# Kernel tuning notes

Hardware: AMD Instinct MI355X
Metric: run time of the kernel (lower is better)

The kernel has to match this reference:

```python
import jax, jax.numpy as jnp
import numpy as np
from jax.scipy.special import logsumexp

B, T, V, C, H, D, SPW, NC = 16, 256, 10000, 4096, 256, 256, 32, 128


def _res(x, w1, b1, w2, b2):
    # ResLayer: x + relu(lin2(relu(lin1(x))))
    return x + jax.nn.relu(jax.nn.relu(x @ w1 + b1) @ w2 + b2)


def _log_phi(x, proj):
    # Performer-style log random features for the softmax kernel (smp param.)
    return x @ proj - 0.5 * jnp.sum(x * x, -1, keepdims=True)


def _log_matmul_exp(a, b):
    # logits[i,j] = logsumexp_d(a[i,d] + b[j,d]), stable, via a single GEMM
    ma = jnp.max(a, -1, keepdims=True)
    mb = jnp.max(b, -1, keepdims=True)
    return jnp.log(jnp.exp(a - ma) @ jnp.exp(b - mb).T) + ma + mb.T


def setup_inputs() -> dict:
    key = jax.random.key(0)
    ks = jax.random.split(key, 12)
    s = 1.0 / np.sqrt(H)  # xavier-ish scale
    inp = {
        "text": jax.random.randint(ks[0], (B, T), 0, V),
        "start_emb": jax.random.normal(ks[1], (H,), jnp.float32) * s,
        "start_w": jax.random.normal(ks[2], (5, H, H), jnp.float32) * s,
        "start_b": jnp.zeros((5, H), jnp.float32),
        "state_emb": jax.random.normal(ks[3], (C, H), jnp.float32) * s,
        "next_state_emb": jax.random.normal(ks[4], (C, H), jnp.float32) * s,
        "preterminal_emb": jax.random.normal(ks[5], (C, H), jnp.float32) * s,
        "terminal_w": jax.random.normal(ks[6], (4, H, H), jnp.float32) * s,
        "terminal_b": jnp.zeros((4, H), jnp.float32),
        "terminal_emb": jax.random.normal(ks[7], (V, H), jnp.float32) * s,
        "projection": jax.random.normal(ks[8], (H, D), jnp.float32),
    }
    # brown-cluster style assignment: each cluster owns SPW disjoint states
    w2c = jax.random.randint(ks[9], (V,), 0, NC)
    c2s = jnp.arange(NC)[:, None] * SPW + jnp.arange(SPW)[None, :]
    inp["word2state"] = c2s[w2c]  # [V, SPW]
    return inp


def reference(text, word2state, start_emb, start_w, start_b, state_emb,
              next_state_emb, preterminal_emb, terminal_w, terminal_b,
              terminal_emb, projection):
    # --- start distribution (tie_start=True uses next_state_emb) ---
    fx = start_emb @ start_w[0] + start_b[0]
    fx = _res(fx, start_w[1], start_b[1], start_w[2], start_b[2])
    fx = _res(fx, start_w[3], start_b[3], start_w[4], start_b[4])
    lpy = _log_phi(next_state_emb, projection)                      # [C, D]
    start_lp = jax.nn.log_softmax(
        _log_matmul_exp(_log_phi(fx[None], projection), lpy)[0])    # [C]
    # --- transition: kernelized low-rank logits, row log-softmax ---
    trans_lp = jax.nn.log_softmax(
        _log_matmul_exp(_log_phi(state_emb, projection), lpy), -1)  # [C, C]
    # --- emission: terminal_mlp + sparse word2state mask ---
    fp = _res(preterminal_emb, terminal_w[0], terminal_b[0], terminal_w[1], terminal_b[1])
    fp = _res(fp, terminal_w[2], terminal_b[2], terminal_w[3], terminal_b[3])
    emit_logits = _log_matmul_exp(_log_phi(fp, projection),
                                  _log_phi(terminal_emb, projection))  # [C, V]
    rows = word2state.reshape(-1)
    cols = jnp.repeat(jnp.arange(V), SPW)
    mask = jnp.zeros((C, V), bool).at[rows, cols].set(True)
    emit_lp = jax.nn.log_softmax(jnp.where(mask, emit_logits, -1e30), -1)
    # --- log-space forward algorithm over clamped sparse states ---
    clamped = word2state[text]                          # [B, T, SPW]
    emit_bt = emit_lp[clamped, text[:, :, None]]        # [B, T, SPW]
    alpha0 = start_lp[clamped[:, 0]] + emit_bt[:, 0]    # [B, SPW]
    xs = (jnp.swapaxes(clamped[:, :-1], 0, 1),
          jnp.swapaxes(clamped[:, 1:], 0, 1),
          jnp.swapaxes(emit_bt[:, 1:], 0, 1))

    def step(alpha, x):
        cp, cc, em = x                                   # [B,SPW] each / em [B,SPW]
        tr = trans_lp[cp[:, :, None], cc[:, None, :]]    # [B, SPW, SPW]
        return logsumexp(alpha[:, :, None] + tr, axis=1) + em, None

    alpha, _ = jax.lax.scan(step, alpha0, xs)
    return logsumexp(alpha, -1)                          # [B] log evidence
```

## Files before the change

kernel.cpp:

```cpp
#include <hip/hip_runtime.h>

#define B_   16
#define T_   256
#define V_   10000
#define C_   4096
#define NC_  128
#define CAP_ 224
#define MST  33
#define HST  264

typedef __bf16 bf16x8 __attribute__((ext_vector_type(8)));
typedef unsigned short u16x8 __attribute__((ext_vector_type(8)));
typedef float  f32x4  __attribute__((ext_vector_type(4)));

__device__ inline unsigned short f2bf(float f){
  unsigned int u = __float_as_uint(f);
  u += 0x7FFFu + ((u >> 16) & 1u);
  return (unsigned short)(u >> 16);
}
__device__ inline float bf2f(unsigned short u){
  return __uint_as_float(((unsigned int)u) << 16);
}
__device__ inline f32x4 mfma16(bf16x8 a, bf16x8 b, f32x4 c){
  return __builtin_amdgcn_mfma_f32_16x16x32_bf16(a, b, c, 0, 0, 0);
}
__device__ inline bf16x8 load_cvt8(const float* p){
  u16x8 u;
  #pragma unroll
  for (int i = 0; i < 8; ++i) u[i] = f2bf(p[i]);
  return __builtin_bit_cast(bf16x8, u);
}
__device__ inline void zero_acc(f32x4 acc[2][4]){
  #pragma unroll
  for (int i = 0; i < 2; ++i)
    #pragma unroll
    for (int jx = 0; jx < 4; ++jx) acc[i][jx] = (f32x4){0.f,0.f,0.f,0.f};
}

__device__ inline void fx_accum(const float* __restrict__ W, const float* xh,
                                int j, float* __restrict__ Anext){
  int t = threadIdx.x;
  float p = 0.f;
  #pragma unroll
  for (int i = 0; i < 8; ++i)
    p = fmaf(xh[i], W[(size_t)(8*j + i)*256 + t], p);
  atomicAdd(&Anext[t], p);
}

__device__ inline void mm_A_gf32(const float* __restrict__ A, size_t lda_row0,
    const unsigned short* __restrict__ Bt, int w, int ln, f32x4 acc[2][4]){
  int m16 = ln & 15, q = ln >> 4, c0 = w*64;
  const float* a0 = A + lda_row0 + (size_t)m16*256 + q*8;
  const float* a1 = a0 + 16*256;
  const unsigned short* bp0 = Bt + (size_t)(c0 + m16)*256 + q*8;
  #pragma unroll
  for (int kt = 0; kt < 8; ++kt){
    bf16x8 af0 = load_cvt8(a0 + kt*32);
    bf16x8 af1 = load_cvt8(a1 + kt*32);
    #pragma unroll
    for (int cj = 0; cj < 4; ++cj){
      bf16x8 bfj = *(const bf16x8*)(bp0 + (size_t)cj*16*256 + kt*32);
      acc[0][cj] = mfma16(af0, bfj, acc[0][cj]);
      acc[1][cj] = mfma16(af1, bfj, acc[1][cj]);
    }
  }
}

__device__ inline void mm_A_ldsbf(const unsigned short* sHb,
    const unsigned short* __restrict__ Bt, int w, int ln, f32x4 acc[2][4]){
  int m16 = ln & 15, q = ln >> 4, c0 = w*64;
  const unsigned short* a0 = sHb + m16*HST + q*8;
  const unsigned short* a1 = sHb + (16 + m16)*HST + q*8;
  const unsigned short* bp0 = Bt + (size_t)(c0 + m16)*256 + q*8;
  #pragma unroll
  for (int kt = 0; kt < 8; ++kt){
    bf16x8 af0 = *(const bf16x8*)(a0 + kt*32);
    bf16x8 af1 = *(const bf16x8*)(a1 + kt*32);
    #pragma unroll
    for (int cj = 0; cj < 4; ++cj){
      bf16x8 bfj = *(const bf16x8*)(bp0 + (size_t)cj*16*256 + kt*32);
      acc[0][cj] = mfma16(af0, bfj, acc[0][cj]);
      acc[1][cj] = mfma16(af1, bfj, acc[1][cj]);
    }
  }
}

__device__ inline void phi_core(const float* __restrict__ A,
    const unsigned short* __restrict__ Bt, int r0, int M, int w, int ln,
    f32x4 acc[2][4], float* lnrm)
{
  int m16 = ln & 15, q = ln >> 4;
  int c0 = w*64;
  int ra0 = r0 + m16;      if (ra0 > M-1) ra0 = M-1;
  int ra1 = r0 + 16 + m16; if (ra1 > M-1) ra1 = M-1;
  const float* a0 = A + (size_t)ra0*256 + q*8;
  const float* a1 = A + (size_t)ra1*256 + q*8;
  const unsigned short* bp0 = Bt + (size_t)(c0 + m16)*256 + q*8;
  float ss0 = 0.f, ss1 = 0.f;
  #pragma unroll
  for (int kt = 0; kt < 8; ++kt){
    float av0[8], av1[8];
    #pragma unroll
    for (int i2 = 0; i2 < 8; ++i2){ av0[i2] = a0[kt*32 + i2]; av1[i2] = a1[kt*32 + i2]; }
    u16x8 u0, u1;
    #pragma unroll
    for (int i2 = 0; i2 < 8; ++i2){
      u0[i2] = f2bf(av0[i2]); u1[i2] = f2bf(av1[i2]);
      ss0 = fmaf(av0[i2], av0[i2], ss0);
      ss1 = fmaf(av1[i2], av1[i2], ss1);
    }
    bf16x8 af0 = __builtin_bit_cast(bf16x8, u0);
    bf16x8 af1 = __builtin_bit_cast(bf16x8, u1);
    #pragma unroll
    for (int cj = 0; cj < 4; ++cj){
      bf16x8 bfj = *(const bf16x8*)(bp0 + (size_t)cj*16*256 + kt*32);
      acc[0][cj] = mfma16(af0, bfj, acc[0][cj]);
      acc[1][cj] = mfma16(af1, bfj, acc[1][cj]);
    }
  }
  ss0 += __shfl_xor(ss0, 16); ss0 += __shfl_xor(ss0, 32);
  ss1 += __shfl_xor(ss1, 16); ss1 += __shfl_xor(ss1, 32);
  if (w == 0 && q == 0){ lnrm[m16] = 0.5f*ss0; lnrm[16 + m16] = 0.5f*ss1; }
}

__device__ inline void dev_phiB(const float* __restrict__ A,
    const unsigned short* __restrict__ projT, unsigned short* __restrict__ Ebp,
    float* __restrict__ S, int r0, float* lnrm)
{
  int tid = threadIdx.x;
  int w = tid >> 6, ln = tid & 63;
  int m16 = ln & 15, q = ln >> 4;
  f32x4 acc[2][4];
  zero_acc(acc);
  phi_core(A, projT, r0, C_, w, ln, acc, lnrm);
  __syncthreads();
  int c0 = w*64;
  #pragma unroll
  for (int cj = 0; cj < 4; ++cj){
    int col = c0 + cj*16 + m16;
    float cs = 0.f;
    #pragma unroll
    for (int ri = 0; ri < 2; ++ri){
      #pragma unroll
      for (int r = 0; r < 4; ++r){
        int row = ri*16 + q*4 + r;
        float e = __expf(acc[ri][cj][r] - lnrm[row]);
        Ebp[(size_t)(r0 + row)*256 + col] = f2bf(e);
        cs += e;
      }
    }
    cs += __shfl_xor(cs, 16); cs += __shfl_xor(cs, 32);
    if (q == 0) atomicAdd(&S[col], cs);
  }
}

__device__ inline void phiE_epilogue(f32x4 acc[2][4], unsigned short* __restrict__ E,
    float* __restrict__ mr, int M, int r0, float* lnrm, float (*wrow)[32])
{
  int tid = threadIdx.x;
  int w = tid >> 6, ln = tid & 63;
  int m16 = ln & 15, q = ln >> 4;
  int c0 = w*64;
  #pragma unroll
  for (int ri = 0; ri < 2; ++ri){
    #pragma unroll
    for (int r = 0; r < 4; ++r){
      int row = ri*16 + q*4 + r;
      float mv = -1e30f;
      #pragma unroll
      for (int cj = 0; cj < 4; ++cj){
        acc[ri][cj][r] -= lnrm[row];
        mv = fmaxf(mv, acc[ri][cj][r]);
      }
      #pragma unroll
      for (int d = 1; d < 16; d <<= 1) mv = fmaxf(mv, __shfl_xor(mv, d));
      if (m16 == 0) wrow[w][row] = mv;
    }
  }
  __syncthreads();
  #pragma unroll
  for (int ri = 0; ri < 2; ++ri){
    #pragma unroll
    for (int r = 0; r < 4; ++r){
      int row = ri*16 + q*4 + r;
      int grow = r0 + row;
      float m = fmaxf(fmaxf(wrow[0][row], wrow[1][row]), fmaxf(wrow[2][row], wrow[3][row]));
      if (grow < M){
        #pragma unroll
        for (int cj = 0; cj < 4; ++cj){
          int col = c0 + cj*16 + m16;
          E[(size_t)grow*256 + col] = f2bf(__expf(acc[ri][cj][r] - m));
        }
        if (w == 0 && m16 == 0) mr[grow] = m;
      }
    }
  }
}

__device__ inline void dev_phiE(const float* __restrict__ A,
    const unsigned short* __restrict__ projT, unsigned short* __restrict__ E,
    float* __restrict__ mr, int M, int r0, float* lnrm, float (*wrow)[32])
{
  int tid = threadIdx.x;
  int w = tid >> 6, ln = tid & 63;
  f32x4 acc[2][4];
  zero_acc(acc);
  phi_core(A, projT, r0, M, w, ln, acc, lnrm);
  __syncthreads();
  phiE_epilogue(acc, E, mr, M, r0, lnrm, wrow);
}

__global__ __launch_bounds__(256) void k_prep(
  const float* __restrict__ proj, const float* __restrict__ tw,
  unsigned short* __restrict__ projT, unsigned short* __restrict__ WT,
  const int* __restrict__ w2s, int* __restrict__ cnt, int* __restrict__ list,
  const float* __restrict__ se, const float* __restrict__ sw,
  float* __restrict__ Afx)
{
  int bx = blockIdx.x, tid = threadIdx.x;
  if (bx < 1280){
    int z = bx >> 8, dcol = bx & 255;
    const float* src = (z == 0) ? proj : (tw + (size_t)(z-1)*65536);
    unsigned short* dst = (z == 0) ? projT : (WT + (size_t)(z-1)*65536);
    dst[dcol*256 + tid] = f2bf(src[tid*256 + dcol]);
    return;
  }
  if (bx < 1320){
    int v = (bx - 1280)*256 + tid;
    if (v < V_){
      int k = w2s[v*32] >> 5;
      int pos = atomicAdd(&cnt[k], 1);
      if (pos < CAP_) list[k*CAP_ + pos] = v;
    }
    return;
  }
  int j = bx - 1320;
  float xh[8];
  #pragma unroll
  for (int i = 0; i < 8; ++i) xh[i] = se[8*j + i];
  fx_accum(sw, xh, j, Afx);
}

__global__ __launch_bounds__(256) void k_stageB(
  const float* __restrict__ pre_emb, const unsigned short* __restrict__ WT,
  const float* __restrict__ term_b,
  const unsigned short* __restrict__ projT,
  unsigned short* __restrict__ Epb, float* __restrict__ mpp,
  const float* __restrict__ next_emb, unsigned short* __restrict__ Ebp,
  float* __restrict__ S,
  const float* __restrict__ term_emb, unsigned short* __restrict__ Etb,
  float* __restrict__ mt,
  const float* __restrict__ sw, const float* __restrict__ sb,
  float* __restrict__ Afx,
  const float* __restrict__ state_emb, unsigned short* __restrict__ Eab,
  float* __restrict__ maS)
{
  __shared__ __align__(16) unsigned short sB1[32*HST];
  __shared__ __align__(16) unsigned short sB2[32*HST];
  __shared__ float lnrm[32];
  __shared__ float wrow[4][32];
  __shared__ float wnorm[4][32];
  int bx = blockIdx.x, tid = threadIdx.x;
  int w = tid >> 6, ln = tid & 63;
  int m16 = ln & 15, q = ln >> 4;
  int c0 = w*64;
  if (bx < 128){
    int r0 = bx*32;
    f32x4 acc[2][4];
    float x2r[2][4][4];
    zero_acc(acc);
    mm_A_gf32(pre_emb, (size_t)r0*256, WT, w, ln, acc);
    #pragma unroll
    for (int ri = 0; ri < 2; ++ri)
      #pragma unroll
      for (int cj = 0; cj < 4; ++cj)
        #pragma unroll
        for (int r = 0; r < 4; ++r){
          int row = ri*16 + q*4 + r, col = c0 + cj*16 + m16;
          sB1[row*HST + col] = f2bf(fmaxf(acc[ri][cj][r] + term_b[col], 0.f));
        }
    __syncthreads();
    zero_acc(acc);
    mm_A_ldsbf(sB1, WT + 65536, w, ln, acc);
    #pragma unroll
    for (int ri = 0; ri < 2; ++ri)
      #pragma unroll
      for (int cj = 0; cj < 4; ++cj)
        #pragma unroll
        for (int r = 0; r < 4; ++r){
          int row = ri*16 + q*4 + r, col = c0 + cj*16 + m16;
          float v = fmaxf(acc[ri][cj][r] + term_b[256 + col], 0.f);
          float x2 = v + pre_emb[(size_t)(r0 + row)*256 + col];
          x2r[ri][cj][r] = x2;
          sB2[row*HST + col] = f2bf(x2);
        }
    __syncthreads();
    zero_acc(acc);
    mm_A_ldsbf(sB2, WT + 2*65536, w, ln, acc);
    __syncthreads();
    #pragma unroll
    for (int ri = 0; ri < 2; ++ri)
      #pragma unroll
      for (int cj = 0; cj < 4; ++cj)
        #pragma unroll
        for (int r = 0; r < 4; ++r){
          int row = ri*16 + q*4 + r, col = c0 + cj*16 + m16;
          sB1[row*HST + col] = f2bf(fmaxf(acc[ri][cj][r] + term_b[512 + col], 0.f));
        }
    __syncthreads();
    zero_acc(acc);
    mm_A_ldsbf(sB1, WT + 3*65536, w, ln, acc);
    __syncthreads();
    #pragma unroll
    for (int ri = 0; ri < 2; ++ri){
      #pragma unroll
      for (int r = 0; r < 4; ++r){
        int row = ri*16 + q*4 + r;
        float ps = 0.f;
        #pragma unroll
        for (int cj = 0; cj < 4; ++cj){
          int col = c0 + cj*16 + m16;
          float x4 = x2r[ri][cj][r] + fmaxf(acc[ri][cj][r] + term_b[768 + col], 0.f);
          sB2[row*HST + col] = f2bf(x4);
          ps = fmaf(x4, x4, ps);
        }
        #pragma unroll
        for (int d = 1; d < 16; d <<= 1) ps += __shfl_xor(ps, d);
        if (m16 == 0) wnorm[w][row] = ps;
      }
    }
    __syncthreads();
    if (tid < 32) lnrm[tid] = 0.5f*(wnorm[0][tid] + wnorm[1][tid] + wnorm[2][tid] + wnorm[3][tid]);
    zero_acc(acc);
    mm_A_ldsbf(sB2, projT, w, ln, acc);
    __syncthreads();
    phiE_epilogue(acc, Epb, mpp, C_, r0, lnrm, wrow);
  } else if (bx < 256){
    dev_phiB(next_emb, projT, Ebp, S, (bx - 128)*32, lnrm);
  } else if (bx < 569){
    dev_phiE(term_emb, projT, Etb, mt, V_, (bx - 256)*32, lnrm, wrow);
  } else if (bx < 601){
    int j = bx - 569;
    float xh[8];
    #pragma unroll
    for (int i = 0; i < 8; ++i){ int h = 8*j + i; xh[i] = Afx[h] + sb[h]; }
    fx_accum(sw + 65536, xh, j, Afx + 256);
  } else {
    dev_phiE(state_emb, projT, Eab, maS, C_, (bx - 601)*32, lnrm, wrow);
  }
}

__global__ __launch_bounds__(256) void k_stageC(
  const unsigned short* __restrict__ Epb, const float* __restrict__ mpp,
  const unsigned short* __restrict__ Etb, const float* __restrict__ mt,
  const int* __restrict__ cnt, const int* __restrict__ list,
  float* __restrict__ emit_col,
  const unsigned short* __restrict__ Eab, const float* __restrict__ S,
  float* __restrict__ denInv,
  const float* __restrict__ sw, const float* __restrict__ sb,
  float* __restrict__ Afx)
{
  __shared__ float mtile[8][32];
  __shared__ float stile[8][32];
  __shared__ float mpl[32];
  __shared__ float denl[32];
  int bx = blockIdx.x, tid = threadIdx.x;
  if (bx >= 192){
    int j = bx - 192;
    float xh[8];
    #pragma unroll
    for (int i = 0; i < 8; ++i){ int h = 8*j + i; xh[i] = fmaxf(Afx[256 + h] + sb[256 + h], 0.f); }
    fx_accum(sw + 2*65536, xh, j, Afx + 512);
    return;
  }
  if (bx >= 128){
    int g = bx - 128;
    int r = g*64 + (tid >> 2);
    int seg = tid & 3;
    const unsigned short* er = Eab + (size_t)r*256 + seg*64;
    const float* sp = S + seg*64;
    float s = 0.f;
    #pragma unroll 8
    for (int i = 0; i < 64; ++i) s = fmaf(bf2f(er[i]), sp[i], s);
    s += __shfl_xor(s, 1);
    s += __shfl_xor(s, 2);
    if (seg == 0) denInv[r] = 1.0f / s;
    return;
  }
  int k = bx;
  int w = tid >> 6, ln = tid & 63;
  int m16 = ln & 15, q = ln >> 4;
  if (tid < 32) mpl[tid] = mpp[k*32 + tid];
  int n = cnt[k]; if (n > CAP_) n = CAP_;
  int nt = (n + 31) >> 5;
  const int* lp = list + k*CAP_;
  bf16x8 af0[8], af1[8];
  {
    const unsigned short* ap0 = Epb + (size_t)(k*32 + m16)*256 + q*8;
    const unsigned short* ap1 = ap0 + 16*256;
    #pragma unroll
    for (int kt = 0; kt < 8; ++kt){
      af0[kt] = *(const bf16x8*)(ap0 + kt*32);
      af1[kt] = *(const bf16x8*)(ap1 + kt*32);
    }
  }
  __syncthreads();
  float lg[2][2][2][4];
  int   vj[2][2];
  #pragma unroll
  for (int u = 0; u < 2; ++u){
    int t = w + u*4;
    if (t >= nt) continue;
    int j0 = t*32 + m16, j1 = j0 + 16;
    int v0 = lp[(j0 < n) ? j0 : 0];
    int v1 = lp[(j1 < n) ? j1 : 0];
    vj[u][0] = v0; vj[u][1] = v1;
    float mt0 = (j0 < n) ? mt[v0] : 0.f;
    float mt1 = (j1 < n) ? mt[v1] : 0.f;
    const unsigned short* bp0 = Etb + (size_t)v0*256 + q*8;
    const unsigned short* bp1 = Etb + (size_t)v1*256 + q*8;
    f32x4 acc[2][2];
    #pragma unroll
    for (int mi = 0; mi < 2; ++mi)
      #pragma unroll
      for (int ni = 0; ni < 2; ++ni) acc[mi][ni] = (f32x4){0.f,0.f,0.f,0.f};
    #pragma unroll
    for (int kt = 0; kt < 8; ++kt){
      bf16x8 b0 = *(const bf16x8*)(bp0 + kt*32);
      bf16x8 b1 = *(const bf16x8*)(bp1 + kt*32);
      acc[0][0] = mfma16(af0[kt], b0, acc[0][0]);
      acc[0][1] = mfma16(af0[kt], b1, acc[0][1]);
      acc[1][0] = mfma16(af1[kt], b0, acc[1][0]);
      acc[1][1] = mfma16(af1[kt], b1, acc[1][1]);
    }
    #pragma unroll
    for (int mi = 0; mi < 2; ++mi){
      #pragma unroll
      for (int r = 0; r < 4; ++r){
        int row = mi*16 + q*4 + r;
        float l0 = (j0 < n) ? (__logf(acc[mi][0][r]) + mpl[row] + mt0) : -1e30f;
        float l1 = (j1 < n) ? (__logf(acc[mi][1][r]) + mpl[row] + mt1) : -1e30f;
        lg[u][mi][0][r] = l0;
        lg[u][mi][1][r] = l1;
        float mv = fmaxf(l0, l1);
        #pragma unroll
        for (int d = 1; d < 16; d <<= 1) mv = fmaxf(mv, __shfl_xor(mv, d));
        float se = __expf(l0 - mv) + __expf(l1 - mv);
        #pragma unroll
        for (int d = 1; d < 16; d <<= 1) se += __shfl_xor(se, d);
        if (m16 == 0){ mtile[t][row] = mv; stile[t][row] = se; }
      }
    }
  }
  __syncthreads();
  if (tid < 32){
    float gm = -1e30f;
    for (int t = 0; t < nt; ++t) gm = fmaxf(gm, mtile[t][tid]);
    float gs = 0.f;
    for (int t = 0; t < nt; ++t) gs += stile[t][tid]*__expf(mtile[t][tid] - gm);
    denl[tid] = gm + __logf(gs);
  }
  __syncthreads();
  #pragma unroll
  for (int u = 0; u < 2; ++u){
    int t = w + u*4;
    if (t >= nt) continue;
    #pragma unroll
    for (int ni = 0; ni < 2; ++ni){
      int j = t*32 + ni*16 + m16;
      if (j >= n) continue;
      float* outp = emit_col + (size_t)vj[u][ni]*32;
      #pragma unroll
      for (int mi = 0; mi < 2; ++mi)
        #pragma unroll
        for (int r = 0; r < 4; ++r){
          int row = mi*16 + q*4 + r;
          outp[row] = lg[u][mi][ni][r] - denl[row];
        }
    }
  }
}

__device__ inline void prod_acc(const float* __restrict__ L0, const float* __restrict__ L1,
                                f32x4 acc[2][2], int ln)
{
  int m16 = ln & 15, q = ln >> 4;
  bf16x8 af[2], bfv[2];
  #pragma unroll
  for (int mi = 0; mi < 2; ++mi){
    const float* p = L0 + (mi*16 + m16)*MST + q*8;
    u16x8 u;
    #pragma unroll
    for (int jj = 0; jj < 8; ++jj) u[jj] = f2bf(p[jj]);
    af[mi] = __builtin_bit_cast(bf16x8, u);
  }
  #pragma unroll
  for (int ni = 0; ni < 2; ++ni){
    u16x8 u;
    #pragma unroll
    for (int jj = 0; jj < 8; ++jj) u[jj] = f2bf(L1[(q*8 + jj)*MST + ni*16 + m16]);
    bfv[ni] = __builtin_bit_cast(bf16x8, u);
  }
  #pragma unroll
  for (int mi = 0; mi < 2; ++mi)
    #pragma unroll
    for (int ni = 0; ni < 2; ++ni) acc[mi][ni] = mfma16(af[mi], bfv[ni], acc[mi][ni]);
}

__device__ inline void wave_norm_store(f32x4 acc[2][2], float* outp,
                                       float sIn, float* sOut, int ln)
{
  int m16 = ln & 15, q = ln >> 4;
  float mx = 0.f;
  #pragma unroll
  for (int mi = 0; mi < 2; ++mi)
    #pragma unroll
    for (int ni = 0; ni < 2; ++ni)
      #pragma unroll
      for (int r = 0; r < 4; ++r) mx = fmaxf(mx, acc[mi][ni][r]);
  #pragma unroll
  for (int d = 1; d < 64; d <<= 1) mx = fmaxf(mx, __shfl_xor(mx, d));
  float inv = 1.0f/mx;
  #pragma unroll
  for (int mi = 0; mi < 2; ++mi)
    #pragma unroll
    for (int ni = 0; ni < 2; ++ni)
      #pragma unroll
      for (int r = 0; r < 4; ++r)
        outp[(mi*16 + q*4 + r)*MST + ni*16 + m16] = acc[mi][ni][r]*inv;
  if (ln == 0) *sOut = sIn + __logf(mx);
}

__device__ inline void norm_store_g16(f32x4 acc[2][2], unsigned short* outp,
                                      float sIn, float* sOutG, int ln)
{
  int m16 = ln & 15, q = ln >> 4;
  float mx = 0.f;
  #pragma unroll
  for (int mi = 0; mi < 2; ++mi)
    #pragma unroll
    for (int ni = 0; ni < 2; ++ni)
      #pragma unroll
      for (int r = 0; r < 4; ++r) mx = fmaxf(mx, acc[mi][ni][r]);
  #pragma unroll
  for (int d = 1; d < 64; d <<= 1) mx = fmaxf(mx, __shfl_xor(mx, d));
  float inv = 1.0f/mx;
  #pragma unroll
  for (int mi = 0; mi < 2; ++mi)
    #pragma unroll
    for (int ni = 0; ni < 2; ++ni)
      #pragma unroll
      for (int r = 0; r < 4; ++r)
        outp[(mi*16 + q*4 + r)*32 + ni*16 + m16] = f2bf(acc[mi][ni][r]*inv);
  if (ln == 0) *sOutG = sIn + __logf(mx);
}

__device__ inline void prod32(const float* L0, const float* L1, float* outp,
                              float sIn, float* sOut, int ln)
{
  f32x4 acc[2][2];
  #pragma unroll
  for (int mi = 0; mi < 2; ++mi)
    #pragma unroll
    for (int ni = 0; ni < 2; ++ni) acc[mi][ni] = (f32x4){0.f,0.f,0.f,0.f};
  prod_acc(L0, L1, acc, ln);
  wave_norm_store(acc, outp, sIn, sOut, ln);
}

__global__ __launch_bounds__(512) void k_chunk(
  const unsigned short* __restrict__ Eab, const unsigned short* __restrict__ Ebp,
  const float* __restrict__ emit_col, const float* __restrict__ denInv,
  const int* __restrict__ text, const int* __restrict__ w2s,
  unsigned short* __restrict__ Gm, float* __restrict__ Gs,
  const float* __restrict__ sw, const float* __restrict__ sb,
  float* __restrict__ Afx)
{
  __shared__ float bufL[8][32*MST];
  __shared__ float bufN[4][32*MST];
  __shared__ float sL[8], sN[4];
  int bx = blockIdx.x;
  int tid = threadIdx.x;
  if (bx >= 512){
    if (tid < 256){
      int j = bx - 512;
      float xh[8];
      #pragma unroll
      for (int i = 0; i < 8; ++i){
        int h = 8*j + i;
        float x0 = Afx[h] + sb[h];
        xh[i] = x0 + fmaxf(Afx[512 + h] + sb[512 + h], 0.f);
      }
      fx_accum(sw + 3*65536, xh, j, Afx + 768);
    }
    return;
  }
  int b = bx >> 5, ch = bx & 31;
  int w = tid >> 6, ln = tid & 63;
  int m16 = ln & 15, q = ln >> 4;
  {
    int s = ch*8 + w;
    float* outp = bufL[w];
    if (s >= 255){
      for (int i = ln; i < 32*32; i += 64){
        int r = i >> 5, c = i & 31;
        outp[r*MST + c] = (r == c) ? 1.f : 0.f;
      }
      if (ln == 0) sL[w] = 0.f;
    } else {
      int vp = text[b*256 + s], vc = text[b*256 + s + 1];
      int bp = w2s[vp*32], bq = w2s[vc*32];
      const unsigned short* a0 = Eab + (size_t)(bp + m16)*256 + q*8;
      const unsigned short* b0 = Ebp + (size_t)(bq + m16)*256 + q*8;
      f32x4 acc[2][2];
      #pragma unroll
      for (int mi = 0; mi < 2; ++mi)
        #pragma unroll
        for (int ni = 0; ni < 2; ++ni) acc[mi][ni] = (f32x4){0.f,0.f,0.f,0.f};
      #pragma unroll
      for (int kt = 0; kt < 8; ++kt){
        bf16x8 a_0 = *(const bf16x8*)(a0 + kt*32);
        bf16x8 a_1 = *(const bf16x8*)(a0 + 16*256 + kt*32);
        bf16x8 b_0 = *(const bf16x8*)(b0 + kt*32);
        bf16x8 b_1 = *(const bf16x8*)(b0 + 16*256 + kt*32);
        acc[0][0] = mfma16(a_0, b_0, acc[0][0]);
        acc[0][1] = mfma16(a_0, b_1, acc[0][1]);
        acc[1][0] = mfma16(a_1, b_0, acc[1][0]);
        acc[1][1] = mfma16(a_1, b_1, acc[1][1]);
      }
      float e0 = __expf(emit_col[(size_t)vc*32 + m16]);
      float e1 = __expf(emit_col[(size_t)vc*32 + 16 + m16]);
      #pragma unroll
      for (int mi = 0; mi < 2; ++mi)
        #pragma unroll
        for (int r = 0; r < 4; ++r){
          float dn = denInv[bp + mi*16 + q*4 + r];
          acc[mi][0][r] *= e0*dn;
          acc[mi][1][r] *= e1*dn;
        }
      wave_norm_store(acc, outp, 0.f, &sL[w], ln);
    }
  }
  __syncthreads();
  if (w < 4) prod32(bufL[2*w], bufL[2*w+1], bufN[w], sL[2*w] + sL[2*w+1], &sN[w], ln);
  __syncthreads();
  if (w < 2) prod32(bufN[2*w], bufN[2*w+1], bufL[w], sN[2*w] + sN[2*w+1], &sL[w], ln);
  __syncthreads();
  if (w == 0){
    f32x4 acc[2][2];
    #pragma unroll
    for (int mi = 0; mi < 2; ++mi)
      #pragma unroll
      for (int ni = 0; ni < 2; ++ni) acc[mi][ni] = (f32x4){0.f,0.f,0.f,0.f};
    prod_acc(bufL[0], bufL[1], acc, ln);
    norm_store_g16(acc, Gm + (size_t)bx*1024, sL[0] + sL[1], Gs + bx, ln);
  }
}

__device__ inline void load_mat16(const unsigned short* __restrict__ g,
                                  float* __restrict__ d, int ln){
  #pragma unroll
  for (int p = 0; p < 16; ++p){
    int idx = p*64 + ln;
    int r = idx >> 5, c = idx & 31;
    d[r*MST + c] = bf2f(g[idx]);
  }
}

__global__ __launch_bounds__(512) void k_root(
  const unsigned short* __restrict__ Gm, const float* __restrict__ Gs,
  const float* __restrict__ Afx, const float* __restrict__ sb,
  const float* __restrict__ sw, const float* __restrict__ proj,
  const float* __restrict__ S,
  const unsigned short* __restrict__ Ebp, const float* __restrict__ emit_col,
  const int* __restrict__ text, const int* __restrict__ w2s, float* __restrict__ out)
{
  __shared__ float W[8][3][32*MST];
  __shared__ float sW[8], sT[1];
  __shared__ float eafx[256], sX2[256], sH[256];
  __shared__ float gpart[2][256];
  __shared__ float red[4];
  int b = blockIdx.x;
  int tid = threadIdx.x;
  int w = tid >> 6, ln = tid & 63;
  int t = tid & 255, u = tid >> 8;
  if (tid < 256){
    float x0 = Afx[tid] + sb[tid];
    sX2[tid] = x0 + fmaxf(Afx[512 + tid] + sb[512 + tid], 0.f);
    sH[tid]  = fmaxf(Afx[768 + tid] + sb[768 + tid], 0.f);
  }
  __syncthreads();
  {
    float a = 0.f;
    const float* Wp = sw + 4*65536 + (size_t)(128*u)*256 + t;
    #pragma unroll 8
    for (int h = 0; h < 128; ++h) a = fmaf(sH[128*u + h], Wp[(size_t)h*256], a);
    gpart[u][t] = a;
  }
  __syncthreads();
  if (tid < 256){
    float A4 = gpart[0][t] + gpart[1][t];
    float x4 = sX2[t] + fmaxf(A4 + sb[1024 + t], 0.f);
    sX2[t] = x4;
    float v2 = x4*x4;
    #pragma unroll
    for (int d = 1; d < 64; d <<= 1) v2 += __shfl_xor(v2, d);
    if ((t & 63) == 0) red[t >> 6] = v2;
  }
  __syncthreads();
  float nx = red[0] + red[1] + red[2] + red[3];
  {
    float a = 0.f;
    const float* Pp = proj + (size_t)(128*u)*256 + t;
    #pragma unroll 8
    for (int h = 0; h < 128; ++h) a = fmaf(sX2[128*u + h], Pp[(size_t)h*256], a);
    gpart[u][t] = a;
  }
  __syncthreads();
  float pxv = 0.f;
  if (tid < 256){
    pxv = gpart[0][t] + gpart[1][t] - 0.5f*nx;
    float m2 = pxv;
    #pragma unroll
    for (int d = 1; d < 64; d <<= 1) m2 = fmaxf(m2, __shfl_xor(m2, d));
    if ((t & 63) == 0) red[t >> 6] = m2;
  }
  __syncthreads();
  float m2g = fmaxf(fmaxf(red[0], red[1]), fmaxf(red[2], red[3]));
  if (tid < 256) eafx[t] = __expf(pxv - m2g);
  __syncthreads();
  const unsigned short* G = Gm + ((size_t)(b*32 + w*4))*1024;
  const float* gs = Gs + b*32 + w*4;
  load_mat16(G,        W[w][0], ln);
  load_mat16(G + 1024, W[w][1], ln);
  prod32(W[w][0], W[w][1], W[w][2], gs[0] + gs[1], &sW[w], ln);
  load_mat16(G + 2048, W[w][0], ln);
  prod32(W[w][2], W[w][0], W[w][1], sW[w] + gs[2], &sW[w], ln);
  load_mat16(G + 3072, W[w][0], ln);
  prod32(W[w][1], W[w][0], W[w][2], sW[w] + gs[3], &sW[w], ln);
  __syncthreads();
  if (w == 0){
    float sAcc = sW[0];
    const float* cur = W[0][2];
    int dsel = 0;
    for (int j = 1; j < 8; ++j){
      float* dst = dsel ? W[0][1] : W[0][0];
      prod32(cur, W[j][2], dst, sAcc + sW[j], &sT[0], ln);
      sAcc = sT[0];
      cur = dst;
      dsel ^= 1;
    }
    float part = 0.f;
    for (int d = ln; d < 256; d += 64) part = fmaf(eafx[d], S[d], part);
    #pragma unroll
    for (int d2 = 1; d2 < 64; d2 <<= 1) part += __shfl_xor(part, d2);
    float dfx = part;
    int v0 = text[b*256];
    int k0 = w2s[v0*32];
    int j = ln & 31, h = ln >> 5;
    const unsigned short* er = Ebp + (size_t)(k0 + j)*256;
    float dot = 0.f;
    for (int d = h*128; d < h*128 + 128; ++d)
      dot = fmaf(eafx[d], bf2f(er[d]), dot);
    dot += __shfl_xor(dot, 32);
    float z0 = __logf(dot) + emit_col[(size_t)v0*32 + j];
    float mz = z0;
    #pragma unroll
    for (int d2 = 1; d2 < 32; d2 <<= 1) mz = fmaxf(mz, __shfl_xor(mz, d2));
    float an = __expf(z0 - mz);
    float cs = 0.f;
    for (int i = h*16; i < h*16 + 16; ++i)
      cs = fmaf(__shfl(an, i), cur[i*MST + j], cs);
    cs += __shfl_xor(cs, 32);
    float tot = cs;
    #pragma unroll
    for (int d2 = 1; d2 < 32; d2 <<= 1) tot += __shfl_xor(tot, d2);
    if (ln == 0) out[b] = __logf(tot) + mz + sAcc - __logf(dfx);
  }
}

extern "C" void kernel_launch(void* const* d_in, const int* in_sizes, int n_in,
                              void* d_out, int out_size, void* d_ws, size_t ws_size,
                              hipStream_t stream)
{
  (void)in_sizes; (void)n_in; (void)out_size; (void)ws_size;
  const int*   text      = (const int*)  d_in[0];
  const float* start_emb = (const float*)d_in[1];
  const float* start_w   = (const float*)d_in[2];
  const float* start_b   = (const float*)d_in[3];
  const float* state_emb = (const float*)d_in[4];
  const float* next_emb  = (const float*)d_in[5];
  const float* pre_emb   = (const float*)d_in[6];
  const float* term_w    = (const float*)d_in[7];
  const float* term_b    = (const float*)d_in[8];
  const float* term_emb  = (const float*)d_in[9];
  const float* proj      = (const float*)d_in[10];
  const int*   w2s       = (const int*)  d_in[11];
  float* out = (float*)d_out;

  char* base = (char*)d_ws;
  size_t off = 0;
  auto alloc = [&](size_t bytes)->char*{
    char* p = base + off;
    off += (bytes + 255) & ~(size_t)255;
    return p;
  };
  int*   cnt = (int*)  alloc(128*4);
  float* Afx = (float*)alloc(4*256*4);
  float* S   = (float*)alloc(256*4);
  unsigned short* projT = (unsigned short*)alloc((size_t)65536*2);
  unsigned short* WT    = (unsigned short*)alloc((size_t)4*65536*2);
  unsigned short* Epb = (unsigned short*)alloc((size_t)C_*256*2);
  float* mpp  = (float*)alloc((size_t)C_*4);
  unsigned short* Etb = (unsigned short*)alloc((size_t)V_*256*2);
  float* mt   = (float*)alloc((size_t)V_*4);
  unsigned short* Eab = (unsigned short*)alloc((size_t)C_*256*2);
  unsigned short* Ebp = (unsigned short*)alloc((size_t)C_*256*2);
  float* maS  = (float*)alloc((size_t)C_*4);
  float* denInv = (float*)alloc((size_t)C_*4);
  int* list = (int*)alloc((size_t)128*CAP_*4);
  float* emit_col = (float*)alloc((size_t)V_*32*4);
  unsigned short* Gm = (unsigned short*)alloc((size_t)512*1024*2);
  float* Gs = (float*)alloc((size_t)512*4);

  (void)hipMemsetAsync(cnt, 0, 512 + 4096 + 1024, stream);

  k_prep<<<1352, 256, 0, stream>>>(proj, term_w, projT, WT, w2s, cnt, list,
                                   start_emb, start_w, Afx);
  k_stageB<<<729, 256, 0, stream>>>(pre_emb, WT, term_b, projT, Epb, mpp,
                                    next_emb, Ebp, S, term_emb, Etb, mt,
                                    start_w, start_b, Afx,
                                    state_emb, Eab, maS);
  k_stageC<<<224, 256, 0, stream>>>(Epb, mpp, Etb, mt, cnt, list, emit_col,
                                    Eab, S, denInv, start_w, start_b, Afx);
  k_chunk<<<544, 512, 0, stream>>>(Eab, Ebp, emit_col, denInv, text, w2s,
                                   Gm, Gs, start_w, start_b, Afx);
  k_root<<<16, 512, 0, stream>>>(Gm, Gs, Afx, start_b, start_w, proj, S,
                                 Ebp, emit_col, text, w2s, out);
}
```

Before: 199.6 us.

## Tile weight transpose through LDS and halve preterminal MLP row tile

The weight and projection transpose in k_prep now moves 32x32 tiles through shared memory, so both reads and writes are coalesced, and the number of blocks drops from 1280 to 320. In k_stageB the preterminal 4-layer MLP chain runs on 16-row tiles instead of 32, which doubles its block count to 256. This shortens the long serial chain each block runs and spreads it over more CUs. In exchange, each block reloads the weight B-operand for half as many rows, so global weight traffic doubles for that branch. The phiE epilogue is inlined for the 16-row case.

```diff
diff --git a/kernel.cpp b/kernel.cpp
--- a/kernel.cpp
+++ b/kernel.cpp
@@ -47,44 +47,6 @@
   atomicAdd(&Anext[t], p);
 }
 
-__device__ inline void mm_A_gf32(const float* __restrict__ A, size_t lda_row0,
-    const unsigned short* __restrict__ Bt, int w, int ln, f32x4 acc[2][4]){
-  int m16 = ln & 15, q = ln >> 4, c0 = w*64;
-  const float* a0 = A + lda_row0 + (size_t)m16*256 + q*8;
-  const float* a1 = a0 + 16*256;
-  const unsigned short* bp0 = Bt + (size_t)(c0 + m16)*256 + q*8;
-  #pragma unroll
-  for (int kt = 0; kt < 8; ++kt){
-    bf16x8 af0 = load_cvt8(a0 + kt*32);
-    bf16x8 af1 = load_cvt8(a1 + kt*32);
-    #pragma unroll
-    for (int cj = 0; cj < 4; ++cj){
-      bf16x8 bfj = *(const bf16x8*)(bp0 + (size_t)cj*16*256 + kt*32);
-      acc[0][cj] = mfma16(af0, bfj, acc[0][cj]);
-      acc[1][cj] = mfma16(af1, bfj, acc[1][cj]);
-    }
-  }
-}
-
-__device__ inline void mm_A_ldsbf(const unsigned short* sHb,
-    const unsigned short* __restrict__ Bt, int w, int ln, f32x4 acc[2][4]){
-  int m16 = ln & 15, q = ln >> 4, c0 = w*64;
-  const unsigned short* a0 = sHb + m16*HST + q*8;
-  const unsigned short* a1 = sHb + (16 + m16)*HST + q*8;
-  const unsigned short* bp0 = Bt + (size_t)(c0 + m16)*256 + q*8;
-  #pragma unroll
-  for (int kt = 0; kt < 8; ++kt){
-    bf16x8 af0 = *(const bf16x8*)(a0 + kt*32);
-    bf16x8 af1 = *(const bf16x8*)(a1 + kt*32);
-    #pragma unroll
-    for (int cj = 0; cj < 4; ++cj){
-      bf16x8 bfj = *(const bf16x8*)(bp0 + (size_t)cj*16*256 + kt*32);
-      acc[0][cj] = mfma16(af0, bfj, acc[0][cj]);
-      acc[1][cj] = mfma16(af1, bfj, acc[1][cj]);
-    }
-  }
-}
-
 __device__ inline void phi_core(const float* __restrict__ A,
     const unsigned short* __restrict__ Bt, int r0, int M, int w, int ln,
     f32x4 acc[2][4], float* lnrm)
@@ -217,16 +179,29 @@
   const float* __restrict__ se, const float* __restrict__ sw,
   float* __restrict__ Afx)
 {
+  __shared__ float ld[32][33];
   int bx = blockIdx.x, tid = threadIdx.x;
-  if (bx < 1280){
-    int z = bx >> 8, dcol = bx & 255;
+  if (bx < 320){
+    int z = bx >> 6, tIdx = bx & 63;
+    int hr = (tIdx >> 3)*32, dc = (tIdx & 7)*32;
     const float* src = (z == 0) ? proj : (tw + (size_t)(z-1)*65536);
     unsigned short* dst = (z == 0) ? projT : (WT + (size_t)(z-1)*65536);
-    dst[dcol*256 + tid] = f2bf(src[tid*256 + dcol]);
+    int lr = tid >> 5, lc = tid & 31;
+    #pragma unroll
+    for (int i = 0; i < 4; ++i){
+      int h = hr + lr + i*8;
+      ld[lr + i*8][lc] = src[(size_t)h*256 + dc + lc];
+    }
+    __syncthreads();
+    #pragma unroll
+    for (int i = 0; i < 4; ++i){
+      int dcol = dc + lr + i*8;
+      dst[(size_t)dcol*256 + hr + lc] = f2bf(ld[lc][lr + i*8]);
+    }
     return;
   }
-  if (bx < 1320){
-    int v = (bx - 1280)*256 + tid;
+  if (bx < 360){
+    int v = (bx - 320)*256 + tid;
     if (v < V_){
       int k = w2s[v*32] >> 5;
       int pos = atomicAdd(&cnt[k], 1);
@@ -234,7 +209,7 @@
     }
     return;
   }
-  int j = bx - 1320;
+  int j = bx - 360;
   float xh[8];
   #pragma unroll
   for (int i = 0; i < 8; ++i) xh[i] = se[8*j + i];
@@ -255,98 +230,167 @@
   const float* __restrict__ state_emb, unsigned short* __restrict__ Eab,
   float* __restrict__ maS)
 {
-  __shared__ __align__(16) unsigned short sB1[32*HST];
-  __shared__ __align__(16) unsigned short sB2[32*HST];
+  __shared__ __align__(16) unsigned short sB1[16*HST];
+  __shared__ __align__(16) unsigned short sB2[16*HST];
   __shared__ float lnrm[32];
   __shared__ float wrow[4][32];
-  __shared__ float wnorm[4][32];
+  __shared__ float wnorm[4][16];
   int bx = blockIdx.x, tid = threadIdx.x;
   int w = tid >> 6, ln = tid & 63;
   int m16 = ln & 15, q = ln >> 4;
   int c0 = w*64;
-  if (bx < 128){
-    int r0 = bx*32;
-    f32x4 acc[2][4];
-    float x2r[2][4][4];
-    zero_acc(acc);
-    mm_A_gf32(pre_emb, (size_t)r0*256, WT, w, ln, acc);
-    #pragma unroll
-    for (int ri = 0; ri < 2; ++ri)
-      #pragma unroll
-      for (int cj = 0; cj < 4; ++cj)
-        #pragma unroll
-        for (int r = 0; r < 4; ++r){
-          int row = ri*16 + q*4 + r, col = c0 + cj*16 + m16;
-          sB1[row*HST + col] = f2bf(fmaxf(acc[ri][cj][r] + term_b[col], 0.f));
-        }
+  if (bx < 256){
+    int r0 = bx*16;
+    f32x4 acc[4];
+    float x2r[4][4];
+    #pragma unroll
+    for (int cj = 0; cj < 4; ++cj) acc[cj] = (f32x4){0.f,0.f,0.f,0.f};
+    {
+      const float* a0 = pre_emb + (size_t)(r0 + m16)*256 + q*8;
+      const unsigned short* bp0 = WT + (size_t)(c0 + m16)*256 + q*8;
+      #pragma unroll
+      for (int kt = 0; kt < 8; ++kt){
+        bf16x8 af = load_cvt8(a0 + kt*32);
+        #pragma unroll
+        for (int cj = 0; cj < 4; ++cj)
+          acc[cj] = mfma16(af, *(const bf16x8*)(bp0 + (size_t)cj*16*256 + kt*32), acc[cj]);
+      }
+    }
+    #pragma unroll
+    for (int cj = 0; cj < 4; ++cj)
+      #pragma unroll
+      for (int r = 0; r < 4; ++r){
+        int row = q*4 + r, col = c0 + cj*16 + m16;
+        sB1[row*HST + col] = f2bf(fmaxf(acc[cj][r] + term_b[col], 0.f));
+      }
     __syncthreads();
-    zero_acc(acc);
-    mm_A_ldsbf(sB1, WT + 65536, w, ln, acc);
-    #pragma unroll
-    for (int ri = 0; ri < 2; ++ri)
-      #pragma unroll
-      for (int cj = 0; cj < 4; ++cj)
-        #pragma unroll
-        for (int r = 0; r < 4; ++r){
-          int row = ri*16 + q*4 + r, col = c0 + cj*16 + m16;
-          float v = fmaxf(acc[ri][cj][r] + term_b[256 + col], 0.f);
-          float x2 = v + pre_emb[(size_t)(r0 + row)*256 + col];
-          x2r[ri][cj][r] = x2;
-          sB2[row*HST + col] = f2bf(x2);
-        }
+    #pragma unroll
+    for (int cj = 0; cj < 4; ++cj) acc[cj] = (f32x4){0.f,0.f,0.f,0.f};
+    {
+      const unsigned short* a0 = sB1 + m16*HST + q*8;
+      const unsigned short* bp0 = WT + 65536 + (size_t)(c0 + m16)*256 + q*8;
+      #pragma unroll
+      for (int kt = 0; kt < 8; ++kt){
+        bf16x8 af = *(const bf16x8*)(a0 + kt*32);
+        #pragma unroll
+        for (int cj = 0; cj < 4; ++cj)
+          acc[cj] = mfma16(af, *(const bf16x8*)(bp0 + (size_t)cj*16*256 + kt*32), acc[cj]);
+      }
+    }
+    #pragma unroll
+    for (int cj = 0; cj < 4; ++cj)
+      #pragma unroll
+      for (int r = 0; r < 4; ++r){
+        int row = q*4 + r, col = c0 + cj*16 + m16;
+        float v = fmaxf(acc[cj][r] + term_b[256 + col], 0.f);
+        float x2 = v + pre_emb[(size_t)(r0 + row)*256 + col];
+        x2r[cj][r] = x2;
+        sB2[row*HST + col] = f2bf(x2);
+      }
     __syncthreads();
-    zero_acc(acc);
-    mm_A_ldsbf(sB2, WT + 2*65536, w, ln, acc);
+    #pragma unroll
+    for (int cj = 0; cj < 4; ++cj) acc[cj] = (f32x4){0.f,0.f,0.f,0.f};
+    {
+      const unsigned short* a0 = sB2 + m16*HST + q*8;
+      const unsigned short* bp0 = WT + 2*65536 + (size_t)(c0 + m16)*256 + q*8;
+      #pragma unroll
+      for (int kt = 0; kt < 8; ++kt){
+        bf16x8 af = *(const bf16x8*)(a0 + kt*32);
+        #pragma unroll
+        for (int cj = 0; cj < 4; ++cj)
+          acc[cj] = mfma16(af, *(const bf16x8*)(bp0 + (size_t)cj*16*256 + kt*32), acc[cj]);
+      }
+    }
+    #pragma unroll
+    for (int cj = 0; cj < 4; ++cj)
+      #pragma unroll
+      for (int r = 0; r < 4; ++r){
+        int row = q*4 + r, col = c0 + cj*16 + m16;
+        sB1[row*HST + col] = f2bf(fmaxf(acc[cj][r] + term_b[512 + col], 0.f));
+      }
     __syncthreads();
     #pragma unroll
-    for (int ri = 0; ri < 2; ++ri)
-      #pragma unroll
-      for (int cj = 0; cj < 4; ++cj)
-        #pragma unroll
-        for (int r = 0; r < 4; ++r){
-          int row = ri*16 + q*4 + r, col = c0 + cj*16 + m16;
-          sB1[row*HST + col] = f2bf(fmaxf(acc[ri][cj][r] + term_b[512 + col], 0.f));
-        }
+    for (int cj = 0; cj < 4; ++cj) acc[cj] = (f32x4){0.f,0.f,0.f,0.f};
+    {
+      const unsigned short* a0 = sB1 + m16*HST + q*8;
+      const unsigned short* bp0 = WT + 3*65536 + (size_t)(c0 + m16)*256 + q*8;
+      #pragma unroll
+      for (int kt = 0; kt < 8; ++kt){
+        bf16x8 af = *(const bf16x8*)(a0 + kt*32);
+        #pragma unroll
+        for (int cj = 0; cj < 4; ++cj)
+          acc[cj] = mfma16(af, *(const bf16x8*)(bp0 + (size_t)cj*16*256 + kt*32), acc[cj]);
+      }
+    }
     __syncthreads();
-    zero_acc(acc);
-    mm_A_ldsbf(sB1, WT + 3*65536, w, ln, acc);
+    #pragma unroll
+    for (int r = 0; r < 4; ++r){
+      int row = q*4 + r;
+      float ps = 0.f;
+      #pragma unroll
+      for (int cj = 0; cj < 4; ++cj){
+        int col = c0 + cj*16 + m16;
+        float x4 = x2r[cj][r] + fmaxf(acc[cj][r] + term_b[768 + col], 0.f);
+        sB2[row*HST + col] = f2bf(x4);
+        ps = fmaf(x4, x4, ps);
+      }
+      #pragma unroll
+      for (int d = 1; d < 16; d <<= 1) ps += __shfl_xor(ps, d);
+      if (m16 == 0) wnorm[w][row] = ps;
+    }
     __syncthreads();
-    #pragma unroll
-    for (int ri = 0; ri < 2; ++ri){
-      #pragma unroll
-      for (int r = 0; r < 4; ++r){
-        int row = ri*16 + q*4 + r;
-        float ps = 0.f;
-        #pragma unroll
-        for (int cj = 0; cj < 4; ++cj){
-          int col = c0 + cj*16 + m16;
-          float x4 = x2r[ri][cj][r] + fmaxf(acc[ri][cj][r] + term_b[768 + col], 0.f);
-          sB2[row*HST + col] = f2bf(x4);
-          ps = fmaf(x4, x4, ps);
-        }
-        #pragma unroll
-        for (int d = 1; d < 16; d <<= 1) ps += __shfl_xor(ps, d);
-        if (m16 == 0) wnorm[w][row] = ps;
+    if (tid < 16) lnrm[tid] = 0.5f*(wnorm[0][tid] + wnorm[1][tid] + wnorm[2][tid] + wnorm[3][tid]);
+    #pragma unroll
+    for (int cj = 0; cj < 4; ++cj) acc[cj] = (f32x4){0.f,0.f,0.f,0.f};
+    {
+      const unsigned short* a0 = sB2 + m16*HST + q*8;
+      const unsigned short* bp0 = projT + (size_t)(c0 + m16)*256 + q*8;
+      #pragma unroll
+      for (int kt = 0; kt < 8; ++kt){
+        bf16x8 af = *(const bf16x8*)(a0 + kt*32);
+        #pragma unroll
+        for (int cj = 0; cj < 4; ++cj)
+          acc[cj] = mfma16(af, *(const bf16x8*)(bp0 + (size_t)cj*16*256 + kt*32), acc[cj]);
       }
     }
     __syncthreads();
-    if (tid < 32) lnrm[tid] = 0.5f*(wnorm[0][tid] + wnorm[1][tid] + wnorm[2][tid] + wnorm[3][tid]);
-    zero_acc(acc);
-    mm_A_ldsbf(sB2, projT, w, ln, acc);
+    #pragma unroll
+    for (int r = 0; r < 4; ++r){
+      int row = q*4 + r;
+      float mv = -1e30f;
+      #pragma unroll
+      for (int cj = 0; cj < 4; ++cj){
+        acc[cj][r] -= lnrm[row];
+        mv = fmaxf(mv, acc[cj][r]);
+      }
+      #pragma unroll
+      for (int d = 1; d < 16; d <<= 1) mv = fmaxf(mv, __shfl_xor(mv, d));
+      if (m16 == 0) wrow[w][row] = mv;
+    }
     __syncthreads();
-    phiE_epilogue(acc, Epb, mpp, C_, r0, lnrm, wrow);
-  } else if (bx < 256){
-    dev_phiB(next_emb, projT, Ebp, S, (bx - 128)*32, lnrm);
-  } else if (bx < 569){
-    dev_phiE(term_emb, projT, Etb, mt, V_, (bx - 256)*32, lnrm, wrow);
-  } else if (bx < 601){
-    int j = bx - 569;
+    #pragma unroll
+    for (int r = 0; r < 4; ++r){
+      int row = q*4 + r, grow = r0 + row;
+      float m = fmaxf(fmaxf(wrow[0][row], wrow[1][row]), fmaxf(wrow[2][row], wrow[3][row]));
+      #pragma unroll
+      for (int cj = 0; cj < 4; ++cj){
+        int col = c0 + cj*16 + m16;
+        Epb[(size_t)grow*256 + col] = f2bf(__expf(acc[cj][r] - m));
+      }
+      if (w == 0 && m16 == 0) mpp[grow] = m;
+    }
+  } else if (bx < 384){
+    dev_phiB(next_emb, projT, Ebp, S, (bx - 256)*32, lnrm);
+  } else if (bx < 697){
+    dev_phiE(term_emb, projT, Etb, mt, V_, (bx - 384)*32, lnrm, wrow);
+  } else if (bx < 729){
+    int j = bx - 697;
     float xh[8];
     #pragma unroll
     for (int i = 0; i < 8; ++i){ int h = 8*j + i; xh[i] = Afx[h] + sb[h]; }
     fx_accum(sw + 65536, xh, j, Afx + 256);
   } else {
-    dev_phiE(state_emb, projT, Eab, maS, C_, (bx - 601)*32, lnrm, wrow);
+    dev_phiE(state_emb, projT, Eab, maS, C_, (bx - 729)*32, lnrm, wrow);
   }
 }
 
@@ -824,9 +868,9 @@
 
   (void)hipMemsetAsync(cnt, 0, 512 + 4096 + 1024, stream);
 
-  k_prep<<<1352, 256, 0, stream>>>(proj, term_w, projT, WT, w2s, cnt, list,
-                                   start_emb, start_w, Afx);
-  k_stageB<<<729, 256, 0, stream>>>(pre_emb, WT, term_b, projT, Epb, mpp,
+  k_prep<<<392, 256, 0, stream>>>(proj, term_w, projT, WT, w2s, cnt, list,
+                                  start_emb, start_w, Afx);
+  k_stageB<<<857, 256, 0, stream>>>(pre_emb, WT, term_b, projT, Epb, mpp,
                                     next_emb, Ebp, S, term_emb, Etb, mt,
                                     start_w, start_b, Afx,
                                     state_emb, Eab, maS);
```

After: 205.5 us. 3.0% more time.
